# Kernel tuning notes

Measured on AMD Instinct MI355X. Metric: run time of the kernel, lower is better.

The kernel has to match this reference:

```python
import jax, jax.numpy as jnp
import numpy as np

D_MODEL = 1024
NUM_HEADS = 16
DEPTH = D_MODEL // NUM_HEADS
B, S = 2, 2048


def setup_inputs() -> dict:
    key = jax.random.key(0)
    ks = jax.random.split(key, 11)
    sc = 1.0 / np.sqrt(D_MODEL)
    inp = {
        "q": jax.random.normal(ks[0], (B, S, D_MODEL), jnp.float32),
        "k": jax.random.normal(ks[1], (B, S, D_MODEL), jnp.float32),
        "v": jax.random.normal(ks[2], (B, S, D_MODEL), jnp.float32),
        # 1 = masked (upper triangle), broadcastable to [B,H,S,S]
        "mask": jnp.triu(jnp.ones((S, S), jnp.float32), k=1)[None, None],
        "wq": jax.random.normal(ks[3], (D_MODEL, D_MODEL), jnp.float32) * sc,
        "bq": jnp.zeros((D_MODEL,), jnp.float32),
        "wk": jax.random.normal(ks[4], (D_MODEL, D_MODEL), jnp.float32) * sc,
        "bk": jnp.zeros((D_MODEL,), jnp.float32),
        "wv": jax.random.normal(ks[5], (D_MODEL, D_MODEL), jnp.float32) * sc,
        "bv": jnp.zeros((D_MODEL,), jnp.float32),
        "wo": jax.random.normal(ks[6], (D_MODEL, D_MODEL), jnp.float32) * sc,
        "bo": jnp.zeros((D_MODEL,), jnp.float32),
    }
    return inp


def _split_heads(x):
    b, s, _ = x.shape
    return x.reshape(b, s, NUM_HEADS, DEPTH).transpose(0, 2, 1, 3)  # [B,H,S,D]


def reference(q, k, v, mask, wq, bq, wk, bk, wv, bv, wo, bo):
    qh = _split_heads(q @ wq + bq)
    kh = _split_heads(k @ wk + bk)
    vh = _split_heads(v @ wv + bv)
    logits = jnp.einsum("bhqd,bhkd->bhqk", qh, kh) / jnp.sqrt(
        jnp.asarray(DEPTH, qh.dtype))
    logits = logits + mask * (-1e9)
    attn = jax.nn.softmax(logits, axis=-1)  # [B,H,S,S]
    ctx = jnp.einsum("bhqk,bhkd->bhqd", attn, vh)
    concat = ctx.transpose(0, 2, 1, 3).reshape(q.shape[0], -1, D_MODEL)
    out = concat @ wo + bo
    return out, attn
```

## Files before the change

### kernel.cpp

```cpp
#include <hip/hip_runtime.h>
#include <cstdint>
#include <cstddef>

#define BATCH   2
#define SEQ     2048
#define DMODEL  1024
#define NHEADS  16
#define DHEAD   64
#define TOKENS  (BATCH*SEQ)

typedef __bf16 bf16_t;
typedef bf16_t bf16x8 __attribute__((ext_vector_type(8)));
typedef bf16_t bf16x4 __attribute__((ext_vector_type(4)));
typedef float  f32x4  __attribute__((ext_vector_type(4)));

__device__ __forceinline__ f32x4 mfma16(bf16x8 a, bf16x8 b, f32x4 c) {
    return __builtin_amdgcn_mfma_f32_16x16x32_bf16(a, b, c, 0, 0, 0);
}

__device__ __forceinline__ void conv_w_body(
    const float* __restrict__ W, bf16_t* __restrict__ Wt)
{
    __shared__ bf16_t tl[64][65];
    const int t  = threadIdx.x;
    const int kb = blockIdx.y * 64;
    const int nb = blockIdx.x * 64;
    const int r  = t >> 2;
    const int cs = (t & 3) * 16;

    const float* src = W + (size_t)(kb + r)*DMODEL + nb + cs;
    #pragma unroll
    for (int j = 0; j < 4; ++j) {
        float4 u = ((const float4*)src)[j];
        tl[r][cs + j*4 + 0] = (bf16_t)u.x;
        tl[r][cs + j*4 + 1] = (bf16_t)u.y;
        tl[r][cs + j*4 + 2] = (bf16_t)u.z;
        tl[r][cs + j*4 + 3] = (bf16_t)u.w;
    }
    __syncthreads();
    bf16_t* dst = Wt + (size_t)(nb + r)*DMODEL + kb + cs;
    #pragma unroll
    for (int h = 0; h < 2; ++h) {
        bf16x8 o;
        #pragma unroll
        for (int j = 0; j < 8; ++j) o[j] = tl[cs + h*8 + j][r];
        *(bf16x8*)(dst + h*8) = o;
    }
}

__global__ __launch_bounds__(256) void conv_w1(
    const float* __restrict__ W, bf16_t* __restrict__ Wt)
{
    conv_w_body(W, Wt);
}

__global__ __launch_bounds__(256) void conv_w3(
    const float* __restrict__ w0, const float* __restrict__ w1,
    const float* __restrict__ w2, bf16_t* __restrict__ t0,
    bf16_t* __restrict__ t1, bf16_t* __restrict__ t2)
{
    const int z = blockIdx.z;
    const float* W  = (z == 0) ? w0 : (z == 1) ? w1 : w2;
    bf16_t*      Wt = (z == 0) ? t0 : (z == 1) ? t1 : t2;
    conv_w_body(W, Wt);
}

__global__ __launch_bounds__(256) void conv_x3(
    const float* __restrict__ x0, const float* __restrict__ x1,
    const float* __restrict__ x2, bf16_t* __restrict__ y0,
    bf16_t* __restrict__ y1, bf16_t* __restrict__ y2)
{
    const int z = blockIdx.z;
    const float* xs = (z == 0) ? x0 : (z == 1) ? x1 : x2;
    bf16_t*      ys = (z == 0) ? y0 : (z == 1) ? y1 : y2;
    const size_t base = ((size_t)blockIdx.x*256 + threadIdx.x) * 8;
    float4 u0 = ((const float4*)(xs + base))[0];
    float4 u1 = ((const float4*)(xs + base))[1];
    bf16x8 vv;
    vv[0]=(bf16_t)u0.x; vv[1]=(bf16_t)u0.y; vv[2]=(bf16_t)u0.z; vv[3]=(bf16_t)u0.w;
    vv[4]=(bf16_t)u1.x; vv[5]=(bf16_t)u1.y; vv[6]=(bf16_t)u1.z; vv[7]=(bf16_t)u1.w;
    *(bf16x8*)(ys + base) = vv;
}

template<int MODE>
__global__ __launch_bounds__(256, 4) void proj_gemm(
    const bf16_t* __restrict__ xin, const bf16_t* __restrict__ Wt,
    const float* __restrict__ bias, void* __restrict__ out)
{
    __shared__ __align__(16) bf16_t Xl[128*72];
    __shared__ __align__(16) bf16_t Wl[64*72];

    const int t    = threadIdx.x;
    const int w    = t >> 6;
    const int lane = t & 63;
    const int quad = lane >> 4;
    const int l16  = lane & 15;
    const int m0   = blockIdx.y * 128;
    const int n0   = blockIdx.x * 64;

    f32x4 acc[2][4] = {};

    for (int kt = 0; kt < DMODEL/64; ++kt) {
        __syncthreads();
        #pragma unroll
        for (int it = 0; it < 4; ++it) {
            int s   = t + it*256;
            int row = s >> 3, seg = s & 7;
            *(bf16x8*)&Xl[row*72 + seg*8] =
                *(const bf16x8*)(xin + (size_t)(m0+row)*DMODEL + kt*64 + seg*8);
        }
        #pragma unroll
        for (int it = 0; it < 2; ++it) {
            int s = t + it*256;
            int n = s >> 3, seg = s & 7;
            *(bf16x8*)&Wl[n*72 + seg*8] =
                *(const bf16x8*)(Wt + (size_t)(n0+n)*DMODEL + kt*64 + seg*8);
        }
        __syncthreads();

        #pragma unroll
        for (int kk = 0; kk < 2; ++kk) {
            bf16x8 a0 = *(const bf16x8*)&Xl[(w*32      + l16)*72 + kk*32 + quad*8];
            bf16x8 a1 = *(const bf16x8*)&Xl[(w*32 + 16 + l16)*72 + kk*32 + quad*8];
            #pragma unroll
            for (int c = 0; c < 4; ++c) {
                bf16x8 b = *(const bf16x8*)&Wl[(c*16 + l16)*72 + kk*32 + quad*8];
                acc[0][c] = mfma16(a0, b, acc[0][c]);
                acc[1][c] = mfma16(a1, b, acc[1][c]);
            }
        }
    }

    #pragma unroll
    for (int r = 0; r < 2; ++r) {
        #pragma unroll
        for (int c = 0; c < 4; ++c) {
            int n = n0 + c*16 + l16;
            float bv = bias[n];
            #pragma unroll
            for (int reg = 0; reg < 4; ++reg) {
                int gm = m0 + w*32 + r*16 + quad*4 + reg;
                float val = acc[r][c][reg] + bv;
                if (MODE == 2) {
                    ((float*)out)[(size_t)gm*DMODEL + n] = val;
                } else {
                    int b = gm >> 11, sTok = gm & (SEQ-1);
                    int h = n >> 6,  d    = n & (DHEAD-1);
                    if (MODE == 0)
                        ((bf16_t*)out)[(((size_t)(b*NHEADS + h))*SEQ + sTok)*DHEAD + d] = (bf16_t)val;
                    else
                        ((bf16_t*)out)[(((size_t)(b*NHEADS + h))*DHEAD + d)*SEQ + sTok] = (bf16_t)val;
                }
            }
        }
    }
}

__global__ __launch_bounds__(256, 4) void attn_kernel(
    const bf16_t* __restrict__ Qh, const bf16_t* __restrict__ Kh,
    const bf16_t* __restrict__ Vt, float* __restrict__ attn,
    bf16_t* __restrict__ ctx)
{
    __shared__ __align__(16) bf16_t Ql[64*72];
    __shared__ __align__(16) bf16_t Kl[64*72];
    __shared__ __align__(16) bf16_t Vl[64*72];
    __shared__ __align__(16) bf16_t Pl[4][16*72];

    const int t    = threadIdx.x;
    const int w    = t >> 6;
    const int lane = t & 63;
    const int quad = lane >> 4;
    const int l16  = lane & 15;
    const int bh   = blockIdx.y;
    const int q0   = (gridDim.x - 1 - blockIdx.x) * 64;

    const bf16_t* Qp = Qh + (size_t)bh * SEQ * DHEAD;
    const bf16_t* Kp = Kh + (size_t)bh * SEQ * DHEAD;
    const bf16_t* Vp = Vt + (size_t)bh * DHEAD * SEQ;
    float* attp = attn + (size_t)bh * SEQ * SEQ;

    #pragma unroll
    for (int it = 0; it < 2; ++it) {
        int s = t + it*256;
        int row = s >> 3, seg = s & 7;
        *(bf16x8*)&Ql[row*72 + seg*8] =
            *(const bf16x8*)(Qp + (size_t)(q0 + row)*DHEAD + seg*8);
    }
    __syncthreads();
    bf16x8 bq[2];
    bq[0] = *(const bf16x8*)&Ql[(w*16 + l16)*72 +      quad*8];
    bq[1] = *(const bf16x8*)&Ql[(w*16 + l16)*72 + 32 + quad*8];

    const int nkt  = q0/64 + 1;
    const int qrow = q0 + w*16 + l16;
    const float C1 = 0.18033688011112042f;

    float m2 = -1e30f, l2 = 0.f;

    for (int kt = 0; kt < nkt; ++kt) {
        __syncthreads();
        #pragma unroll
        for (int it = 0; it < 2; ++it) {
            int s = t + it*256;
            int row = s >> 3, seg = s & 7;
            *(bf16x8*)&Kl[row*72 + seg*8] =
                *(const bf16x8*)(Kp + (size_t)(kt*64 + row)*DHEAD + seg*8);
        }
        __syncthreads();

        f32x4 sf[4] = {};
        #pragma unroll
        for (int kk = 0; kk < 2; ++kk) {
            #pragma unroll
            for (int c = 0; c < 4; ++c) {
                bf16x8 ak = *(const bf16x8*)&Kl[(c*16 + l16)*72 + kk*32 + quad*8];
                sf[c] = mfma16(ak, bq[kk], sf[c]);
            }
        }
        float tm = -1e30f;
        if (kt == nkt - 1) {
            #pragma unroll
            for (int c = 0; c < 4; ++c) {
                int colb = kt*64 + c*16 + quad*4;
                #pragma unroll
                for (int reg = 0; reg < 4; ++reg) {
                    float z = sf[c][reg] * C1;
                    z = (colb + reg > qrow) ? -1e30f : z;
                    sf[c][reg] = z;
                    tm = fmaxf(tm, z);
                }
            }
        } else {
            #pragma unroll
            for (int c = 0; c < 4; ++c)
                #pragma unroll
                for (int reg = 0; reg < 4; ++reg) {
                    float z = sf[c][reg] * C1;
                    sf[c][reg] = z;
                    tm = fmaxf(tm, z);
                }
        }
        tm = fmaxf(tm, __shfl_xor(tm, 16));
        tm = fmaxf(tm, __shfl_xor(tm, 32));
        float mnew = fmaxf(m2, tm);
        float ps = 0.f;
        #pragma unroll
        for (int c = 0; c < 4; ++c)
            #pragma unroll
            for (int reg = 0; reg < 4; ++reg)
                ps += exp2f(sf[c][reg] - mnew);
        ps += __shfl_xor(ps, 16);
        ps += __shfl_xor(ps, 32);
        l2 = l2 * exp2f(m2 - mnew) + ps;
        m2 = mnew;
    }
    const float invl = 1.0f / l2;

    f32x4 cacc[4] = {};
    bf16_t* Plw = &Pl[w][0];

    for (int kt = 0; kt < nkt; ++kt) {
        __syncthreads();
        #pragma unroll
        for (int it = 0; it < 2; ++it) {
            int s = t + it*256;
            int row = s >> 3, seg = s & 7;
            *(bf16x8*)&Kl[row*72 + seg*8] =
                *(const bf16x8*)(Kp + (size_t)(kt*64 + row)*DHEAD + seg*8);
            *(bf16x8*)&Vl[row*72 + seg*8] =
                *(const bf16x8*)(Vp + (size_t)row*SEQ + kt*64 + seg*8);
        }
        __syncthreads();

        f32x4 sf[4] = {};
        #pragma unroll
        for (int kk = 0; kk < 2; ++kk) {
            #pragma unroll
            for (int c = 0; c < 4; ++c) {
                bf16x8 ak = *(const bf16x8*)&Kl[(c*16 + l16)*72 + kk*32 + quad*8];
                sf[c] = mfma16(ak, bq[kk], sf[c]);
            }
        }
        const bool diag = (kt == nkt - 1);
        #pragma unroll
        for (int c = 0; c < 4; ++c) {
            int colb = kt*64 + c*16 + quad*4;
            f32x4 pv;
            if (diag) {
                #pragma unroll
                for (int reg = 0; reg < 4; ++reg) {
                    float z = sf[c][reg] * C1;
                    pv[reg] = (colb + reg > qrow) ? 0.0f : exp2f(z - m2) * invl;
                }
            } else {
                #pragma unroll
                for (int reg = 0; reg < 4; ++reg)
                    pv[reg] = exp2f(sf[c][reg] * C1 - m2) * invl;
            }
            *(f32x4*)(attp + (size_t)qrow*SEQ + colb) = pv;
            bf16x4 pk;
            pk[0]=(bf16_t)pv[0]; pk[1]=(bf16_t)pv[1];
            pk[2]=(bf16_t)pv[2]; pk[3]=(bf16_t)pv[3];
            *(bf16x4*)&Plw[l16*72 + c*16 + quad*4] = pk;
        }
        #pragma unroll
        for (int kk = 0; kk < 2; ++kk) {
            bf16x8 ap = *(const bf16x8*)&Plw[l16*72 + kk*32 + quad*8];
            #pragma unroll
            for (int c = 0; c < 4; ++c) {
                bf16x8 bv = *(const bf16x8*)&Vl[(c*16 + l16)*72 + kk*32 + quad*8];
                cacc[c] = mfma16(ap, bv, cacc[c]);
            }
        }
    }

    {
        const int r = t >> 2;
        const int c4base = nkt*16 + (t & 3);
        f32x4 z = {0.f, 0.f, 0.f, 0.f};
        float* rowp = attp + (size_t)(q0 + r)*SEQ;
        for (int c4 = c4base; c4 < SEQ/4; c4 += 4)
            ((f32x4*)rowp)[c4] = z;
    }

    const int b = bh >> 4, h = bh & 15;
    #pragma unroll
    for (int c = 0; c < 4; ++c) {
        #pragma unroll
        for (int reg = 0; reg < 4; ++reg) {
            int gq = q0 + w*16 + quad*4 + reg;
            size_t idx = ((size_t)(b*SEQ + gq))*DMODEL + h*DHEAD + c*16 + l16;
            ctx[idx] = (bf16_t)cacc[c][reg];
        }
    }
}

extern "C" void kernel_launch(void* const* d_in, const int* in_sizes, int n_in,
                              void* d_out, int out_size, void* d_ws, size_t ws_size,
                              hipStream_t stream) {
    const float* q  = (const float*)d_in[0];
    const float* k  = (const float*)d_in[1];
    const float* v  = (const float*)d_in[2];
    const float* wq = (const float*)d_in[4];
    const float* bq = (const float*)d_in[5];
    const float* wk = (const float*)d_in[6];
    const float* bk = (const float*)d_in[7];
    const float* wv = (const float*)d_in[8];
    const float* bv = (const float*)d_in[9];
    const float* wo = (const float*)d_in[10];
    const float* bo = (const float*)d_in[11];

    float* out  = (float*)d_out;
    float* attn = out + (size_t)TOKENS * DMODEL;

    bf16_t* Qws = (bf16_t*)d_ws;
    bf16_t* Kws = Qws + (size_t)TOKENS * DMODEL;
    bf16_t* Vws = Kws + (size_t)TOKENS * DMODEL;
    bf16_t* Cws = Vws + (size_t)TOKENS * DMODEL;

    const size_t WSZ = (size_t)DMODEL*DMODEL;
    const size_t XSZ = (size_t)TOKENS*DMODEL;
    bf16_t* WtQ = (bf16_t*)attn;
    bf16_t* WtK = WtQ + WSZ;
    bf16_t* WtV = WtK + WSZ;
    bf16_t* Xq  = WtV + WSZ;
    bf16_t* Xk  = Xq + XSZ;
    bf16_t* Xv  = Xk + XSZ;
    bf16_t* WtO = Qws;

    dim3 blk(256);
    dim3 gconvw(DMODEL/64, DMODEL/64, 3);
    dim3 gconvx(XSZ/8/256, 1, 3);
    dim3 gproj(DMODEL/64, TOKENS/128);

    conv_w3<<<gconvw, blk, 0, stream>>>(wq, wk, wv, WtQ, WtK, WtV);
    conv_x3<<<gconvx, blk, 0, stream>>>(q, k, v, Xq, Xk, Xv);
    proj_gemm<0><<<gproj, blk, 0, stream>>>(Xq, WtQ, bq, Qws);
    proj_gemm<0><<<gproj, blk, 0, stream>>>(Xk, WtK, bk, Kws);
    proj_gemm<1><<<gproj, blk, 0, stream>>>(Xv, WtV, bv, Vws);

    dim3 gattn(SEQ/64, BATCH*NHEADS);
    attn_kernel<<<gattn, blk, 0, stream>>>(Qws, Kws, Vws, attn, Cws);

    dim3 gconvw1(DMODEL/64, DMODEL/64);
    conv_w1<<<gconvw1, blk, 0, stream>>>(wo, WtO);
    proj_gemm<2><<<gproj, blk, 0, stream>>>(Cws, WtO, bo, out);
}
```

Measured before the change: 900.5 us.

## Pair causal query tiles per attention block and batch QKV projections

After: 809.9 us. -10.1%, faster.

```diff
diff --git a/kernel.cpp b/kernel.cpp
--- a/kernel.cpp
+++ b/kernel.cpp
@@ -82,13 +82,22 @@
     *(bf16x8*)(ys + base) = vv;
 }
 
-template<int MODE>
-__global__ __launch_bounds__(256, 4) void proj_gemm(
-    const bf16_t* __restrict__ xin, const bf16_t* __restrict__ Wt,
-    const float* __restrict__ bias, void* __restrict__ out)
+__global__ __launch_bounds__(256, 4) void proj_qkv(
+    const bf16_t* __restrict__ Xq, const bf16_t* __restrict__ Xk,
+    const bf16_t* __restrict__ Xv, const bf16_t* __restrict__ WtQ,
+    const bf16_t* __restrict__ WtK, const bf16_t* __restrict__ WtV,
+    const float* __restrict__ bq, const float* __restrict__ bk,
+    const float* __restrict__ bv, bf16_t* __restrict__ Qo,
+    bf16_t* __restrict__ Ko, bf16_t* __restrict__ Vo)
 {
     __shared__ __align__(16) bf16_t Xl[128*72];
     __shared__ __align__(16) bf16_t Wl[64*72];
+
+    const int z = blockIdx.z;
+    const bf16_t* xin  = (z == 0) ? Xq  : (z == 1) ? Xk  : Xv;
+    const bf16_t* Wt   = (z == 0) ? WtQ : (z == 1) ? WtK : WtV;
+    const float*  bias = (z == 0) ? bq  : (z == 1) ? bk  : bv;
+    bf16_t*       out  = (z == 0) ? Qo  : (z == 1) ? Ko  : Vo;
 
     const int t    = threadIdx.x;
     const int w    = t >> 6;
@@ -131,48 +140,119 @@
         }
     }
 
+    const bool vmode = (z == 2);
     #pragma unroll
     for (int r = 0; r < 2; ++r) {
         #pragma unroll
         for (int c = 0; c < 4; ++c) {
             int n = n0 + c*16 + l16;
-            float bv = bias[n];
+            float bv_ = bias[n];
+            int h = n >> 6, d = n & (DHEAD-1);
             #pragma unroll
             for (int reg = 0; reg < 4; ++reg) {
                 int gm = m0 + w*32 + r*16 + quad*4 + reg;
-                float val = acc[r][c][reg] + bv;
-                if (MODE == 2) {
-                    ((float*)out)[(size_t)gm*DMODEL + n] = val;
-                } else {
-                    int b = gm >> 11, sTok = gm & (SEQ-1);
-                    int h = n >> 6,  d    = n & (DHEAD-1);
-                    if (MODE == 0)
-                        ((bf16_t*)out)[(((size_t)(b*NHEADS + h))*SEQ + sTok)*DHEAD + d] = (bf16_t)val;
-                    else
-                        ((bf16_t*)out)[(((size_t)(b*NHEADS + h))*DHEAD + d)*SEQ + sTok] = (bf16_t)val;
-                }
-            }
-        }
-    }
-}
-
-__global__ __launch_bounds__(256, 4) void attn_kernel(
-    const bf16_t* __restrict__ Qh, const bf16_t* __restrict__ Kh,
-    const bf16_t* __restrict__ Vt, float* __restrict__ attn,
-    bf16_t* __restrict__ ctx)
-{
-    __shared__ __align__(16) bf16_t Ql[64*72];
-    __shared__ __align__(16) bf16_t Kl[64*72];
-    __shared__ __align__(16) bf16_t Vl[64*72];
-    __shared__ __align__(16) bf16_t Pl[4][16*72];
+                float val = acc[r][c][reg] + bv_;
+                int b = gm >> 11, sTok = gm & (SEQ-1);
+                if (!vmode)
+                    out[(((size_t)(b*NHEADS + h))*SEQ + sTok)*DHEAD + d] = (bf16_t)val;
+                else
+                    out[(((size_t)(b*NHEADS + h))*DHEAD + d)*SEQ + sTok] = (bf16_t)val;
+            }
+        }
+    }
+}
+
+__global__ __launch_bounds__(256, 4) void proj_out(
+    const bf16_t* __restrict__ xin, const bf16_t* __restrict__ Wt,
+    const float* __restrict__ bias, float* __restrict__ out)
+{
+    __shared__ __align__(16) bf16_t Xl[128*72];
+    __shared__ __align__(16) bf16_t Wl[64*72];
 
     const int t    = threadIdx.x;
     const int w    = t >> 6;
     const int lane = t & 63;
     const int quad = lane >> 4;
     const int l16  = lane & 15;
-    const int bh   = blockIdx.y;
-    const int q0   = (gridDim.x - 1 - blockIdx.x) * 64;
+    const int m0   = blockIdx.y * 128;
+    const int n0   = blockIdx.x * 64;
+
+    f32x4 acc[2][4] = {};
+
+    for (int kt = 0; kt < DMODEL/64; ++kt) {
+        __syncthreads();
+        #pragma unroll
+        for (int it = 0; it < 4; ++it) {
+            int s   = t + it*256;
+            int row = s >> 3, seg = s & 7;
+            *(bf16x8*)&Xl[row*72 + seg*8] =
+                *(const bf16x8*)(xin + (size_t)(m0+row)*DMODEL + kt*64 + seg*8);
+        }
+        #pragma unroll
+        for (int it = 0; it < 2; ++it) {
+            int s = t + it*256;
+            int n = s >> 3, seg = s & 7;
+            *(bf16x8*)&Wl[n*72 + seg*8] =
+                *(const bf16x8*)(Wt + (size_t)(n0+n)*DMODEL + kt*64 + seg*8);
+        }
+        __syncthreads();
+
+        #pragma unroll
+        for (int kk = 0; kk < 2; ++kk) {
+            bf16x8 a0 = *(const bf16x8*)&Xl[(w*32      + l16)*72 + kk*32 + quad*8];
+            bf16x8 a1 = *(const bf16x8*)&Xl[(w*32 + 16 + l16)*72 + kk*32 + quad*8];
+            #pragma unroll
+            for (int c = 0; c < 4; ++c) {
+                bf16x8 b = *(const bf16x8*)&Wl[(c*16 + l16)*72 + kk*32 + quad*8];
+                acc[0][c] = mfma16(a0, b, acc[0][c]);
+                acc[1][c] = mfma16(a1, b, acc[1][c]);
+            }
+        }
+    }
+
+    #pragma unroll
+    for (int r = 0; r < 2; ++r) {
+        #pragma unroll
+        for (int c = 0; c < 4; ++c) {
+            int n = n0 + c*16 + l16;
+            float bv = bias[n];
+            #pragma unroll
+            for (int reg = 0; reg < 4; ++reg) {
+                int gm = m0 + w*32 + r*16 + quad*4 + reg;
+                out[(size_t)gm*DMODEL + n] = acc[r][c][reg] + bv;
+            }
+        }
+    }
+}
+
+__global__ __launch_bounds__(512, 4) void attn_kernel(
+    const bf16_t* __restrict__ Qh, const bf16_t* __restrict__ Kh,
+    const bf16_t* __restrict__ Vt, float* __restrict__ attn,
+    bf16_t* __restrict__ ctx)
+{
+    __shared__ __align__(16) bf16_t Ql[2][64*72];
+    __shared__ __align__(16) bf16_t Kl[64*72];
+    __shared__ __align__(16) bf16_t Vl[64*72];
+    __shared__ __align__(16) bf16_t Pl[8][16*72];
+
+    const int t    = threadIdx.x;
+    const int w    = t >> 6;
+    const int lane = t & 63;
+    const int quad = lane >> 4;
+    const int l16  = lane & 15;
+    const int grp  = w >> 2;
+    const int wg   = w & 3;
+
+    const int bid = blockIdx.x;
+    const int pp  = bid & 15;
+    const int bh  = bid >> 4;
+    const int p   = (bh & 16) ? (15 - pp) : pp;
+    const int qtA = p, qtB = 31 - p;
+    const int nktA = qtA + 1;
+    const int nktB = qtB + 1;
+    const int qt   = grp ? qtB : qtA;
+    const int q0   = qt * 64;
+    const int nkt  = qt + 1;
 
     const bf16_t* Qp = Qh + (size_t)bh * SEQ * DHEAD;
     const bf16_t* Kp = Kh + (size_t)bh * SEQ * DHEAD;
@@ -181,90 +261,89 @@
 
     #pragma unroll
     for (int it = 0; it < 2; ++it) {
-        int s = t + it*256;
+        int s = t + it*512;
         int row = s >> 3, seg = s & 7;
-        *(bf16x8*)&Ql[row*72 + seg*8] =
-            *(const bf16x8*)(Qp + (size_t)(q0 + row)*DHEAD + seg*8);
+        int tl = row >> 6, r = row & 63;
+        int gq = (tl ? qtB : qtA)*64 + r;
+        *(bf16x8*)&Ql[tl][r*72 + seg*8] =
+            *(const bf16x8*)(Qp + (size_t)gq*DHEAD + seg*8);
     }
     __syncthreads();
     bf16x8 bq[2];
-    bq[0] = *(const bf16x8*)&Ql[(w*16 + l16)*72 +      quad*8];
-    bq[1] = *(const bf16x8*)&Ql[(w*16 + l16)*72 + 32 + quad*8];
-
-    const int nkt  = q0/64 + 1;
-    const int qrow = q0 + w*16 + l16;
+    bq[0] = *(const bf16x8*)&Ql[grp][(wg*16 + l16)*72 +      quad*8];
+    bq[1] = *(const bf16x8*)&Ql[grp][(wg*16 + l16)*72 + 32 + quad*8];
+
+    const int qrow = q0 + wg*16 + l16;
     const float C1 = 0.18033688011112042f;
 
     float m2 = -1e30f, l2 = 0.f;
 
-    for (int kt = 0; kt < nkt; ++kt) {
-        __syncthreads();
-        #pragma unroll
-        for (int it = 0; it < 2; ++it) {
-            int s = t + it*256;
-            int row = s >> 3, seg = s & 7;
+    for (int kt = 0; kt < nktB; ++kt) {
+        __syncthreads();
+        {
+            int row = t >> 3, seg = t & 7;
             *(bf16x8*)&Kl[row*72 + seg*8] =
                 *(const bf16x8*)(Kp + (size_t)(kt*64 + row)*DHEAD + seg*8);
         }
         __syncthreads();
 
-        f32x4 sf[4] = {};
-        #pragma unroll
-        for (int kk = 0; kk < 2; ++kk) {
-            #pragma unroll
-            for (int c = 0; c < 4; ++c) {
-                bf16x8 ak = *(const bf16x8*)&Kl[(c*16 + l16)*72 + kk*32 + quad*8];
-                sf[c] = mfma16(ak, bq[kk], sf[c]);
-            }
-        }
-        float tm = -1e30f;
-        if (kt == nkt - 1) {
-            #pragma unroll
-            for (int c = 0; c < 4; ++c) {
-                int colb = kt*64 + c*16 + quad*4;
-                #pragma unroll
-                for (int reg = 0; reg < 4; ++reg) {
-                    float z = sf[c][reg] * C1;
-                    z = (colb + reg > qrow) ? -1e30f : z;
-                    sf[c][reg] = z;
-                    tm = fmaxf(tm, z);
+        if (kt < nkt) {
+            f32x4 sf[4] = {};
+            #pragma unroll
+            for (int kk = 0; kk < 2; ++kk) {
+                #pragma unroll
+                for (int c = 0; c < 4; ++c) {
+                    bf16x8 ak = *(const bf16x8*)&Kl[(c*16 + l16)*72 + kk*32 + quad*8];
+                    sf[c] = mfma16(ak, bq[kk], sf[c]);
                 }
             }
-        } else {
+            float tm = -1e30f;
+            if (kt == nkt - 1) {
+                #pragma unroll
+                for (int c = 0; c < 4; ++c) {
+                    int colb = kt*64 + c*16 + quad*4;
+                    #pragma unroll
+                    for (int reg = 0; reg < 4; ++reg) {
+                        float zv = sf[c][reg] * C1;
+                        zv = (colb + reg > qrow) ? -1e30f : zv;
+                        sf[c][reg] = zv;
+                        tm = fmaxf(tm, zv);
+                    }
+                }
+            } else {
+                #pragma unroll
+                for (int c = 0; c < 4; ++c)
+                    #pragma unroll
+                    for (int reg = 0; reg < 4; ++reg) {
+                        float zv = sf[c][reg] * C1;
+                        sf[c][reg] = zv;
+                        tm = fmaxf(tm, zv);
+                    }
+            }
+            tm = fmaxf(tm, __shfl_xor(tm, 16));
+            tm = fmaxf(tm, __shfl_xor(tm, 32));
+            float mnew = fmaxf(m2, tm);
+            float ps = 0.f;
             #pragma unroll
             for (int c = 0; c < 4; ++c)
                 #pragma unroll
-                for (int reg = 0; reg < 4; ++reg) {
-                    float z = sf[c][reg] * C1;
-                    sf[c][reg] = z;
-                    tm = fmaxf(tm, z);
-                }
-        }
-        tm = fmaxf(tm, __shfl_xor(tm, 16));
-        tm = fmaxf(tm, __shfl_xor(tm, 32));
-        float mnew = fmaxf(m2, tm);
-        float ps = 0.f;
-        #pragma unroll
-        for (int c = 0; c < 4; ++c)
-            #pragma unroll
-            for (int reg = 0; reg < 4; ++reg)
-                ps += exp2f(sf[c][reg] - mnew);
-        ps += __shfl_xor(ps, 16);
-        ps += __shfl_xor(ps, 32);
-        l2 = l2 * exp2f(m2 - mnew) + ps;
-        m2 = mnew;
+                for (int reg = 0; reg < 4; ++reg)
+                    ps += exp2f(sf[c][reg] - mnew);
+            ps += __shfl_xor(ps, 16);
+            ps += __shfl_xor(ps, 32);
+            l2 = l2 * exp2f(m2 - mnew) + ps;
+            m2 = mnew;
+        }
     }
     const float invl = 1.0f / l2;
 
     f32x4 cacc[4] = {};
     bf16_t* Plw = &Pl[w][0];
 
-    for (int kt = 0; kt < nkt; ++kt) {
-        __syncthreads();
-        #pragma unroll
-        for (int it = 0; it < 2; ++it) {
-            int s = t + it*256;
-            int row = s >> 3, seg = s & 7;
+    for (int kt = 0; kt < nktB; ++kt) {
+        __syncthreads();
+        {
+            int row = t >> 3, seg = t & 7;
             *(bf16x8*)&Kl[row*72 + seg*8] =
                 *(const bf16x8*)(Kp + (size_t)(kt*64 + row)*DHEAD + seg*8);
             *(bf16x8*)&Vl[row*72 + seg*8] =
@@ -272,55 +351,59 @@
         }
         __syncthreads();
 
-        f32x4 sf[4] = {};
-        #pragma unroll
-        for (int kk = 0; kk < 2; ++kk) {
+        if (kt < nkt) {
+            f32x4 sf[4] = {};
+            #pragma unroll
+            for (int kk = 0; kk < 2; ++kk) {
+                #pragma unroll
+                for (int c = 0; c < 4; ++c) {
+                    bf16x8 ak = *(const bf16x8*)&Kl[(c*16 + l16)*72 + kk*32 + quad*8];
+                    sf[c] = mfma16(ak, bq[kk], sf[c]);
+                }
+            }
+            const bool diag = (kt == nkt - 1);
             #pragma unroll
             for (int c = 0; c < 4; ++c) {
-                bf16x8 ak = *(const bf16x8*)&Kl[(c*16 + l16)*72 + kk*32 + quad*8];
-                sf[c] = mfma16(ak, bq[kk], sf[c]);
-            }
-        }
-        const bool diag = (kt == nkt - 1);
-        #pragma unroll
-        for (int c = 0; c < 4; ++c) {
-            int colb = kt*64 + c*16 + quad*4;
-            f32x4 pv;
-            if (diag) {
-                #pragma unroll
-                for (int reg = 0; reg < 4; ++reg) {
-                    float z = sf[c][reg] * C1;
-                    pv[reg] = (colb + reg > qrow) ? 0.0f : exp2f(z - m2) * invl;
+                int colb = kt*64 + c*16 + quad*4;
+                f32x4 pv;
+                if (diag) {
+                    #pragma unroll
+                    for (int reg = 0; reg < 4; ++reg) {
+                        float zv = sf[c][reg] * C1;
+                        pv[reg] = (colb + reg > qrow) ? 0.0f : exp2f(zv - m2) * invl;
+                    }
+                } else {
+                    #pragma unroll
+                    for (int reg = 0; reg < 4; ++reg)
+                        pv[reg] = exp2f(sf[c][reg] * C1 - m2) * invl;
                 }
-            } else {
-                #pragma unroll
-                for (int reg = 0; reg < 4; ++reg)
-                    pv[reg] = exp2f(sf[c][reg] * C1 - m2) * invl;
-            }
-            *(f32x4*)(attp + (size_t)qrow*SEQ + colb) = pv;
-            bf16x4 pk;
-            pk[0]=(bf16_t)pv[0]; pk[1]=(bf16_t)pv[1];
-            pk[2]=(bf16_t)pv[2]; pk[3]=(bf16_t)pv[3];
-            *(bf16x4*)&Plw[l16*72 + c*16 + quad*4] = pk;
-        }
-        #pragma unroll
-        for (int kk = 0; kk < 2; ++kk) {
-            bf16x8 ap = *(const bf16x8*)&Plw[l16*72 + kk*32 + quad*8];
-            #pragma unroll
-            for (int c = 0; c < 4; ++c) {
-                bf16x8 bv = *(const bf16x8*)&Vl[(c*16 + l16)*72 + kk*32 + quad*8];
-                cacc[c] = mfma16(ap, bv, cacc[c]);
+                *(f32x4*)(attp + (size_t)qrow*SEQ + colb) = pv;
+                bf16x4 pk;
+                pk[0]=(bf16_t)pv[0]; pk[1]=(bf16_t)pv[1];
+                pk[2]=(bf16_t)pv[2]; pk[3]=(bf16_t)pv[3];
+                *(bf16x4*)&Plw[l16*72 + c*16 + quad*4] = pk;
+            }
+            #pragma unroll
+            for (int kk = 0; kk < 2; ++kk) {
+                bf16x8 ap = *(const bf16x8*)&Plw[l16*72 + kk*32 + quad*8];
+                #pragma unroll
+                for (int c = 0; c < 4; ++c) {
+                    bf16x8 bv = *(const bf16x8*)&Vl[(c*16 + l16)*72 + kk*32 + quad*8];
+                    cacc[c] = mfma16(ap, bv, cacc[c]);
+                }
             }
         }
     }
 
     {
-        const int r = t >> 2;
-        const int c4base = nkt*16 + (t & 3);
-        f32x4 z = {0.f, 0.f, 0.f, 0.f};
-        float* rowp = attp + (size_t)(q0 + r)*SEQ;
-        for (int c4 = c4base; c4 < SEQ/4; c4 += 4)
-            ((f32x4*)rowp)[c4] = z;
+        const int zq0  = (grp ? qtB : qtA) * 64;
+        const int znkt = grp ? nktB : nktA;
+        const int r    = (t & 255) >> 2;
+        const int c4b  = znkt*16 + (t & 3);
+        f32x4 zz = {0.f, 0.f, 0.f, 0.f};
+        float* rowp = attp + (size_t)(zq0 + r)*SEQ;
+        for (int c4 = c4b; c4 < SEQ/4; c4 += 4)
+            ((f32x4*)rowp)[c4] = zz;
     }
 
     const int b = bh >> 4, h = bh & 15;
@@ -328,7 +411,7 @@
     for (int c = 0; c < 4; ++c) {
         #pragma unroll
         for (int reg = 0; reg < 4; ++reg) {
-            int gq = q0 + w*16 + quad*4 + reg;
+            int gq = q0 + wg*16 + quad*4 + reg;
             size_t idx = ((size_t)(b*SEQ + gq))*DMODEL + h*DHEAD + c*16 + l16;
             ctx[idx] = (bf16_t)cacc[c][reg];
         }
@@ -371,18 +454,18 @@
     dim3 blk(256);
     dim3 gconvw(DMODEL/64, DMODEL/64, 3);
     dim3 gconvx(XSZ/8/256, 1, 3);
-    dim3 gproj(DMODEL/64, TOKENS/128);
+    dim3 gproj(DMODEL/64, TOKENS/128, 3);
 
     conv_w3<<<gconvw, blk, 0, stream>>>(wq, wk, wv, WtQ, WtK, WtV);
     conv_x3<<<gconvx, blk, 0, stream>>>(q, k, v, Xq, Xk, Xv);
-    proj_gemm<0><<<gproj, blk, 0, stream>>>(Xq, WtQ, bq, Qws);
-    proj_gemm<0><<<gproj, blk, 0, stream>>>(Xk, WtK, bk, Kws);
-    proj_gemm<1><<<gproj, blk, 0, stream>>>(Xv, WtV, bv, Vws);
-
-    dim3 gattn(SEQ/64, BATCH*NHEADS);
-    attn_kernel<<<gattn, blk, 0, stream>>>(Qws, Kws, Vws, attn, Cws);
+    proj_qkv<<<gproj, blk, 0, stream>>>(Xq, Xk, Xv, WtQ, WtK, WtV,
+                                        bq, bk, bv, Qws, Kws, Vws);
+
+    dim3 gattn(512);
+    attn_kernel<<<gattn, dim3(512), 0, stream>>>(Qws, Kws, Vws, attn, Cws);
 
     dim3 gconvw1(DMODEL/64, DMODEL/64);
     conv_w1<<<gconvw1, blk, 0, stream>>>(wo, WtO);
-    proj_gemm<2><<<gproj, blk, 0, stream>>>(Cws, WtO, bo, out);
-}
+    dim3 gout(DMODEL/64, TOKENS/128);
+    proj_out<<<gout, blk, 0, stream>>>(Cws, WtO, bo, out);
+}
```
